# Kernel tuning notes

Measured on AMD Instinct MI355X. Metric: run time of the kernel, lower is better.

Reference implementation:

```python
import jax, jax.numpy as jnp
import numpy as np
from jax import lax

B, N, D, L, EDGE_H, NGNN = 8, 128, 256, 64, 64, 3


def setup_inputs() -> dict:
    key = jax.random.key(0)
    ks = iter(jax.random.split(key, 64))
    def nrm(shape, s=0.02):
        return jax.random.normal(next(ks), shape, jnp.float32) * s
    inp = {}
    inp["node_feats"] = jax.random.uniform(next(ks), (B, N, 11), jnp.float32)
    inp["edge_feats"] = jax.random.normal(next(ks), (B, N, N, 3), jnp.float32)
    inp["adj_mask"] = jax.random.randint(next(ks), (B, N, N), 0, 2).astype(bool)
    inp["layer_costs"] = jax.random.uniform(next(ks), (B, L), jnp.float32)
    inp["global_dynamic"] = jax.random.uniform(next(ks), (B, 2), jnp.float32)
    inp["p_node_w"] = nrm((11, D)); inp["p_node_b"] = jnp.zeros((D,), jnp.float32)
    inp["g_w1"] = nrm((NGNN, D + 3, EDGE_H)); inp["g_b1"] = jnp.zeros((NGNN, EDGE_H), jnp.float32)
    inp["g_w2"] = nrm((NGNN, EDGE_H, D)); inp["g_b2"] = jnp.zeros((NGNN, D), jnp.float32)
    inp["u_w1"] = nrm((NGNN, 3 * D, D)); inp["u_b1"] = jnp.zeros((NGNN, D), jnp.float32)
    inp["u_w2"] = nrm((NGNN, D, D)); inp["u_b2"] = jnp.zeros((NGNN, D), jnp.float32)
    inp["ln_g"] = jnp.ones((NGNN, D), jnp.float32); inp["ln_b"] = jnp.zeros((NGNN, D), jnp.float32)
    inp["conv_w"] = nrm((32, 1, 4)); inp["conv_b"] = jnp.zeros((32,), jnp.float32)
    inp["lp_w"] = nrm((32 * 31, D)); inp["lp_b"] = jnp.zeros((D,), jnp.float32)
    inp["q_w"] = nrm((2 * D + 2, D)); inp["q_b"] = jnp.zeros((D,), jnp.float32)
    inp["k_w"] = nrm((D, D)); inp["k_b"] = jnp.zeros((D,), jnp.float32)
    inp["s_w1"] = nrm((D + 2, D)); inp["s_b1"] = jnp.zeros((D,), jnp.float32)
    inp["s_w2"] = nrm((D, 1)); inp["s_b2"] = jnp.zeros((1,), jnp.float32)
    inp["v_w1"] = nrm((2 * D + 2, D)); inp["v_b1"] = jnp.zeros((D,), jnp.float32)
    inp["v_w2"] = nrm((D, 1)); inp["v_b2"] = jnp.zeros((1,), jnp.float32)
    return inp


def _ecgc(h, edge_feats, adj_bool, gw1, gb1, gw2, gb2, uw1, ub1, uw2, ub2, lng, lnb):
    Bh, Nn, Dd = h.shape
    # h_j: features of sender node j broadcast over receiver axis -> (B, N, N, D)
    h_j = jnp.broadcast_to(h[:, None, :, :], (Bh, Nn, Nn, Dd))
    gate_in = jnp.concatenate([h_j, edge_feats], axis=-1)            # (B,N,N,D+3)
    gates = jax.nn.sigmoid(jax.nn.relu(gate_in @ gw1 + gb1) @ gw2 + gb2)
    msg = gates * h_j                                                # (B,N,N,D)
    m = adj_bool.astype(h.dtype)[..., None]
    cnt = jnp.maximum(m.sum(axis=2), 1.0)                            # (B,N,1)
    agg_mean = (msg * m).sum(axis=2) / cnt                           # (B,N,D)
    agg_max = jnp.where(adj_bool[..., None], msg, -jnp.inf).max(axis=2)
    agg_max = jnp.where(jnp.isinf(agg_max), 0.0, agg_max)
    ui = jnp.concatenate([h, agg_mean, agg_max], axis=-1)            # (B,N,3D)
    x = h + (jax.nn.relu(ui @ uw1 + ub1) @ uw2 + ub2)
    mu = x.mean(-1, keepdims=True)
    var = ((x - mu) ** 2).mean(-1, keepdims=True)
    return (x - mu) * lax.rsqrt(var + 1e-5) * lng + lnb


def reference(node_feats, edge_feats, adj_mask, layer_costs, global_dynamic,
              p_node_w, p_node_b, g_w1, g_b1, g_w2, g_b2, u_w1, u_b1, u_w2, u_b2,
              ln_g, ln_b, conv_w, conv_b, lp_w, lp_b, q_w, q_b, k_w, k_b,
              s_w1, s_b1, s_w2, s_b2, v_w1, v_b1, v_w2, v_b2):
    # layer cost encoder: Conv1d(1,32,k=4,s=2) + ReLU, flatten, Linear
    le = lax.conv_general_dilated(layer_costs[:, None, :], conv_w, (2,), 'VALID',
                                  dimension_numbers=('NCH', 'OIH', 'NCH'))
    le = jax.nn.relu(le + conv_b[None, :, None])                     # (B,32,31)
    layer_embed = le.reshape(le.shape[0], -1) @ lp_w + lp_b          # (B,D)
    h = node_feats @ p_node_w + p_node_b                             # (B,N,D)
    for i in range(g_w1.shape[0]):
        h = _ecgc(h, edge_feats, adj_mask, g_w1[i], g_b1[i], g_w2[i], g_b2[i],
                  u_w1[i], u_b1[i], u_w2[i], u_b2[i], ln_g[i], ln_b[i])
    w = (node_feats[:, :, 0] * node_feats[:, :, 7])[..., None]       # (B,N,1)
    graph_embed = (w * h).sum(axis=1) / jnp.maximum(w.sum(axis=1), 1e-8)
    qi = jnp.concatenate([graph_embed, layer_embed, global_dynamic], axis=-1)
    query = qi @ q_w + q_b                                           # (B,D)
    keys = h @ k_w + k_b                                             # (B,N,D)
    device_scores = jnp.einsum('bnd,bd->bn', keys, query) / jnp.sqrt(jnp.float32(query.shape[-1]))
    si = jnp.concatenate([graph_embed, global_dynamic], axis=-1)
    stop_logit = jax.nn.relu(si @ s_w1 + s_b1) @ s_w2 + s_b2         # (B,1)
    all_logits = jnp.concatenate([device_scores, stop_logit], axis=1)
    value = jax.nn.relu(qi @ v_w1 + v_b1) @ v_w2 + v_b2              # (B,1)
    return all_logits, value, h
```

## Files before the change

kernel.cpp:

```cpp
#include <hip/hip_runtime.h>
#include <hip/hip_bf16.h>
#include <math.h>

#define BB 8
#define NN_ 128
#define DD 256
#define LL 64
#define EH 64
#define NG 3

typedef __attribute__((ext_vector_type(8))) short bs8;
typedef __attribute__((ext_vector_type(4))) float f4;

__device__ __forceinline__ short f2bf(float f) {
    __hip_bfloat16 h = __float2bfloat16(f);
    return *reinterpret_cast<short*>(&h);
}

__device__ __forceinline__ bs8 cvt8(const float* __restrict__ p) {
    bs8 r;
    #pragma unroll
    for (int i = 0; i < 8; ++i) r[i] = f2bf(p[i]);
    return r;
}

__device__ __forceinline__ float blockReduceSum(float v, float* sRed) {
    int tid = threadIdx.x;
    __syncthreads();
    sRed[tid] = v;
    __syncthreads();
    for (int s = 128; s > 0; s >>= 1) {
        if (tid < s) sRed[tid] += sRed[tid + s];
        __syncthreads();
    }
    return sRed[0];
}

__global__ __launch_bounds__(256) void k_prep(
    const float* __restrict__ uw1, const float* __restrict__ uw2,
    const float* __restrict__ gw2, const float* __restrict__ gw1,
    const float* __restrict__ kw, const unsigned char* __restrict__ adj,
    const float* __restrict__ lc, const float* __restrict__ cw,
    const float* __restrict__ cb, const float* __restrict__ lpw,
    unsigned short* __restrict__ w1t, unsigned short* __restrict__ w2t,
    unsigned short* __restrict__ g2t, unsigned short* __restrict__ g1t,
    unsigned short* __restrict__ kwt, int* __restrict__ mode,
    float* __restrict__ lpart)
{
    const int blk = blockIdx.x, tid = threadIdx.x;
    if (blk == 232) {
        __shared__ int sOff, sBig;
        if (tid == 0) { sOff = 0; sBig = 0; }
        __syncthreads();
        int off = 0, big = 0;
        #pragma unroll
        for (int k = 0; k < 4; ++k) {
            unsigned char v = adj[tid * 4 + k];
            if (v > 1) big = 1;
            if (k != 0 && v != 0) off = 1;
        }
        if (off) atomicOr(&sOff, 1);
        if (big) atomicOr(&sBig, 1);
        __syncthreads();
        if (tid == 0) mode[0] = sBig ? 2 : (sOff ? 0 : 1);
        return;
    }
    if (blk > 232) {
        const int lb = blk - 233;
        const int b = lb >> 5, kseg = (lb >> 2) & 7, c4 = lb & 3;
        const int d = tid & 63, ss = tid >> 6;
        __shared__ float sC[LL];
        __shared__ float sV[124];
        __shared__ float sP[4][64];
        if (tid < LL) sC[tid] = lc[b * LL + tid];
        __syncthreads();
        if (tid < 124) {
            int idx = kseg * 124 + tid;
            int c = idx / 31, t = idx - c * 31;
            float a = cb[c];
            #pragma unroll
            for (int k = 0; k < 4; ++k) a += sC[2 * t + k] * cw[c * 4 + k];
            sV[tid] = fmaxf(a, 0.f);
        }
        __syncthreads();
        float acc = 0.f;
        for (int k = ss; k < 124; k += 4)
            acc += sV[k] * lpw[(size_t)(kseg * 124 + k) * DD + c4 * 64 + d];
        sP[ss][d] = acc;
        __syncthreads();
        if (ss == 0)
            lpart[(b * 32 + kseg * 4 + c4) * 64 + d] = sP[0][d] + sP[1][d] + sP[2][d] + sP[3][d];
        return;
    }
    const float* src; unsigned short* dst; int K, kt, dt, srcw = 256;
    if (blk < 144)      { int l = blk / 48, t = blk % 48; kt = t >> 2; dt = t & 3;
                          src = uw1 + (size_t)l * 196608; dst = w1t + (size_t)l * 196608; K = 768; }
    else if (blk < 192) { int x = blk - 144, l = x / 16, t = x % 16; kt = t >> 2; dt = t & 3;
                          src = uw2 + (size_t)l * 65536; dst = w2t + (size_t)l * 65536; K = 256; }
    else if (blk < 204) { int x = blk - 192, l = x >> 2; kt = 0; dt = x & 3;
                          src = gw2 + (size_t)l * 16384; dst = g2t + (size_t)l * 16384; K = 64; }
    else if (blk < 216) { int x = blk - 204, l = x >> 2; kt = x & 3; dt = 0; srcw = 64;
                          src = gw1 + (size_t)l * 16576; dst = g1t + (size_t)l * 16384; K = 256; }
    else                { int x = blk - 216; kt = x >> 2; dt = x & 3;
                          src = kw; dst = kwt; K = 256; }
    __shared__ float sT[64][65];
    #pragma unroll
    for (int q = 0; q < 16; ++q) {
        int idx = q * 256 + tid, kk = idx >> 6, dd = idx & 63;
        sT[kk][dd] = src[(size_t)(kt * 64 + kk) * srcw + dt * 64 + dd];
    }
    __syncthreads();
    const int d = tid >> 2, kc = (tid & 3) * 16;
    unsigned short* drow = dst + (size_t)(dt * 64 + d) * K + kt * 64 + kc;
    #pragma unroll
    for (int i = 0; i < 16; ++i) drow[i] = (unsigned short)f2bf(sT[kc + i][d]);
}

__global__ __launch_bounds__(256) void k_npp(
    const float* __restrict__ nf, const float* __restrict__ pnw,
    const float* __restrict__ pnb,
    const unsigned short* __restrict__ g1t, const float* __restrict__ gb1,
    float* __restrict__ h, float* __restrict__ preg)
{
    const int tid = threadIdx.x, blk = blockIdx.x;
    const int row0 = blk * 16;
    const int lane = tid & 63, w = tid >> 6;
    const int lcol = lane & 15, lrow = lane >> 4;
    __shared__ float sF[16][12];
    __shared__ float sH[16][260];
    if (tid < 176) sF[tid / 11][tid % 11] = nf[(size_t)(row0 + tid / 11) * 11 + tid % 11];
    __syncthreads();
    float acc[16];
    {
        float bb = pnb[tid];
        #pragma unroll
        for (int rr = 0; rr < 16; ++rr) acc[rr] = bb;
    }
    #pragma unroll
    for (int f = 0; f < 11; ++f) {
        float wf = pnw[f * DD + tid];
        #pragma unroll
        for (int rr = 0; rr < 16; ++rr) acc[rr] += sF[rr][f] * wf;
    }
    #pragma unroll
    for (int rr = 0; rr < 16; ++rr) {
        sH[rr][tid] = acc[rr];
        h[(size_t)(row0 + rr) * DD + tid] = acc[rr];
    }
    __syncthreads();
    const unsigned short* bR = g1t + (size_t)(w * 16 + lcol) * 256;
    f4 a2 = {0.f, 0.f, 0.f, 0.f};
    #pragma unroll
    for (int ks = 0; ks < 8; ++ks) {
        int k0 = ks * 32 + lrow * 8;
        bs8 av = cvt8(&sH[lcol][k0]);
        bs8 bv = *(const bs8*)(bR + k0);
        a2 = __builtin_amdgcn_mfma_f32_16x16x32_bf16(av, bv, a2, 0, 0, 0);
    }
    const float gb = gb1[w * 16 + lcol];
    #pragma unroll
    for (int r = 0; r < 4; ++r)
        preg[(size_t)(row0 + lrow * 4 + r) * EH + w * 16 + lcol] = a2[r] + gb;
}

__global__ __launch_bounds__(256) void k_edge(
    const float* __restrict__ h, const float* __restrict__ preg,
    const float* __restrict__ edge, const void* __restrict__ adj,
    const int* __restrict__ mode,
    const float* __restrict__ gw1,
    const unsigned short* __restrict__ g2t,
    const float* __restrict__ gb2,
    float* __restrict__ agg_mean, float* __restrict__ agg_max)
{
    const int tid = threadIdx.x;
    const int bi = blockIdx.x;
    const int b = bi >> 7;
    const int lane = tid & 63, w = tid >> 6;
    const int lrow = lane >> 4, lcol = lane & 15;
    const int md = mode[0];

    __shared__ __align__(16) unsigned int sHid[4096];
    __shared__ float sWe[192];
    __shared__ float sE[384];
    __shared__ unsigned long long sMask[2];

    if (tid < 192) sWe[tid] = gw1[16384 + tid];
    const float* eB = edge + (size_t)bi * 384;
    for (int idx = tid; idx < 384; idx += 256) sE[idx] = eB[idx];
    if (tid < 128) {
        int mv;
        if (md == 1)      mv = ((const int*)adj)[(size_t)bi * NN_ + tid] != 0;
        else if (md == 2) mv = ((const float*)adj)[(size_t)bi * NN_ + tid] != 0.f;
        else              mv = ((const unsigned char*)adj)[(size_t)bi * NN_ + tid] != 0;
        unsigned long long bal = __ballot(mv);
        if ((tid & 63) == 0) sMask[tid >> 6] = bal;
    }
    __syncthreads();

    const float* pB = preg + (size_t)b * NN_ * EH;
    #pragma unroll
    for (int q = 0; q < 16; ++q) {
        int idx = q * 256 + tid;
        int j = idx >> 5, p = idx & 31;
        float2 pv = *(const float2*)(pB + j * EH + 2 * p);
        float e0 = sE[j * 3], e1 = sE[j * 3 + 1], e2 = sE[j * 3 + 2];
        int t0 = 2 * p, t1 = t0 + 1;
        float v0 = fmaxf(pv.x + e0 * sWe[t0] + e1 * sWe[64 + t0] + e2 * sWe[128 + t0], 0.f);
        float v1 = fmaxf(pv.y + e0 * sWe[t1] + e1 * sWe[64 + t1] + e2 * sWe[128 + t1], 0.f);
        unsigned int pk = (unsigned int)(unsigned short)f2bf(v0) |
                          ((unsigned int)(unsigned short)f2bf(v1) << 16);
        sHid[j * 32 + (p ^ ((j & 7) << 2))] = pk;
    }
    __syncthreads();

    const unsigned long long m0 = sMask[0], m1 = sMask[1];
    const float cntf = (float)(__popcll(m0) + __popcll(m1));

    bs8 bfr[4][2];
    float bg[4];
    #pragma unroll
    for (int nt = 0; nt < 4; ++nt) {
        int d = w * 64 + nt * 16 + lcol;
        bg[nt] = gb2[d];
        #pragma unroll
        for (int ks = 0; ks < 2; ++ks) {
            int k0 = ks * 32 + lrow * 8;
            bfr[nt][ks] = *(const bs8*)(g2t + (size_t)d * 64 + k0);
        }
    }

    const float* hB = h + (size_t)b * NN_ * DD;
    float vs[4] = {0.f, 0.f, 0.f, 0.f};
    float vm[4] = {-INFINITY, -INFINITY, -INFINITY, -INFINITY};

    #pragma unroll
    for (int pp = 0; pp < 2; ++pp) {
        f4 acc[4][4] = {};
        #pragma unroll
        for (int ks = 0; ks < 2; ++ks) {
            bs8 afr[4];
            #pragma unroll
            for (int m = 0; m < 4; ++m) {
                int j = pp * 64 + m * 16 + lcol;
                int k0 = ks * 32 + lrow * 8;
                afr[m] = *(const bs8*)(sHid + (j * 32 + ((k0 >> 1) ^ ((j & 7) << 2))));
            }
            #pragma unroll
            for (int m = 0; m < 4; ++m)
                #pragma unroll
                for (int nt = 0; nt < 4; ++nt)
                    acc[m][nt] = __builtin_amdgcn_mfma_f32_16x16x32_bf16(
                        afr[m], bfr[nt][ks], acc[m][nt], 0, 0, 0);
        }
        const unsigned long long mw = pp ? m1 : m0;
        #pragma unroll
        for (int m = 0; m < 4; ++m) {
            #pragma unroll
            for (int nt = 0; nt < 4; ++nt) {
                int dnt = w * 64 + nt * 16 + lcol;
                #pragma unroll
                for (int r = 0; r < 4; ++r) {
                    int bit = m * 16 + lrow * 4 + r;
                    float x = acc[m][nt][r] + bg[nt];
                    float g = __builtin_amdgcn_rcpf(1.0f + __expf(-x));
                    float msg = g * hB[(pp * 64 + bit) * DD + dnt];
                    int on = (int)((mw >> bit) & 1ULL);
                    vs[nt] += on ? msg : 0.f;
                    vm[nt] = fmaxf(vm[nt], on ? msg : -INFINITY);
                }
            }
        }
    }

    #pragma unroll
    for (int nt = 0; nt < 4; ++nt) {
        float s = vs[nt];
        s += __shfl_xor(s, 16); s += __shfl_xor(s, 32);
        vs[nt] = s;
        float m = vm[nt];
        m = fmaxf(m, __shfl_xor(m, 16)); m = fmaxf(m, __shfl_xor(m, 32));
        vm[nt] = m;
    }
    const int g = lrow;
    float ssel = (g == 0) ? vs[0] : (g == 1) ? vs[1] : (g == 2) ? vs[2] : vs[3];
    float msel = (g == 0) ? vm[0] : (g == 1) ? vm[1] : (g == 2) ? vm[2] : vm[3];
    const int d = w * 64 + lane;
    agg_mean[(size_t)bi * DD + d] = ssel / fmaxf(cntf, 1.f);
    agg_max[(size_t)bi * DD + d] = (cntf > 0.f) ? msel : 0.f;
}

__global__ __launch_bounds__(256) void k_updp(
    const float* __restrict__ h, const float* __restrict__ amean,
    const float* __restrict__ amax,
    const unsigned short* __restrict__ w1t,
    const float* __restrict__ ub1,
    const unsigned short* __restrict__ w2t,
    const float* __restrict__ ub2,
    const float* __restrict__ lng, const float* __restrict__ lnb,
    float* __restrict__ hout, float* __restrict__ out2,
    const unsigned short* __restrict__ g1tn, const float* __restrict__ gb1n,
    float* __restrict__ preg)
{
    const int tid = threadIdx.x;
    const int row0 = blockIdx.x * 4;
    const int lane = tid & 63, w = tid >> 6;
    const int lcol = lane & 15, lrow = lane >> 4;

    __shared__ __align__(16) unsigned int sX32[16 * 384];
    __shared__ __align__(16) unsigned short sH16[16 * 256];
    __shared__ float sRes[4][256];
    __shared__ float sOut[4][260];

    {
        const int j = w;
        const float* hR = h + (size_t)(row0 + j) * DD;
        const float* mR = amean + (size_t)(row0 + j) * DD;
        const float* xR = amax + (size_t)(row0 + j) * DD;
        #pragma unroll
        for (int q = 0; q < 6; ++q) {
            int p = lane + q * 64;
            int k = 2 * p;
            float2 v;
            if (k < 256)      { v = *(const float2*)(hR + k); sRes[j][k] = v.x; sRes[j][k + 1] = v.y; }
            else if (k < 512)   v = *(const float2*)(mR + (k - 256));
            else                v = *(const float2*)(xR + (k - 512));
            unsigned int pk = (unsigned int)(unsigned short)f2bf(v.x) |
                              ((unsigned int)(unsigned short)f2bf(v.y) << 16);
            sX32[j * 384 + (p ^ (j << 2))] = pk;
        }
    }
    __syncthreads();

    const char* sXb = (const char*)sX32;
    const unsigned short* w1r = w1t + (size_t)(w * 64 + lcol) * 768;
    f4 a0 = {0.f, 0.f, 0.f, 0.f}, a1 = a0, a2 = a0, a3 = a0;
    #pragma unroll 4
    for (int ks = 0; ks < 24; ++ks) {
        int k0 = ks * 32 + lrow * 8;
        bs8 av = *(const bs8*)(sXb + lcol * 1536 + ((((k0 >> 3) ^ (lcol & 7))) << 4));
        bs8 b0 = *(const bs8*)(w1r + k0);
        bs8 b1 = *(const bs8*)(w1r + 16 * 768 + k0);
        bs8 b2 = *(const bs8*)(w1r + 32 * 768 + k0);
        bs8 b3 = *(const bs8*)(w1r + 48 * 768 + k0);
        a0 = __builtin_amdgcn_mfma_f32_16x16x32_bf16(av, b0, a0, 0, 0, 0);
        a1 = __builtin_amdgcn_mfma_f32_16x16x32_bf16(av, b1, a1, 0, 0, 0);
        a2 = __builtin_amdgcn_mfma_f32_16x16x32_bf16(av, b2, a2, 0, 0, 0);
        a3 = __builtin_amdgcn_mfma_f32_16x16x32_bf16(av, b3, a3, 0, 0, 0);
    }
    if (lrow == 0) {
        #pragma unroll
        for (int nt = 0; nt < 4; ++nt) {
            int d = w * 64 + nt * 16 + lcol;
            float bb = ub1[d];
            f4 A = (nt == 0) ? a0 : (nt == 1) ? a1 : (nt == 2) ? a2 : a3;
            #pragma unroll
            for (int r = 0; r < 4; ++r) {
                float hv = fmaxf(A[r] + bb, 0.f);
                sH16[r * 256 + (d ^ (r << 3))] = (unsigned short)f2bf(hv);
            }
        }
    }
    __syncthreads();

    const unsigned short* w2r = w2t + (size_t)(w * 64 + lcol) * 256;
    f4 c0 = {0.f, 0.f, 0.f, 0.f}, c1 = c0, c2 = c0, c3 = c0;
    #pragma unroll
    for (int ks = 0; ks < 8; ++ks) {
        int k0 = ks * 32 + lrow * 8;
        bs8 av = *(const bs8*)((const char*)sH16 + lcol * 512 + ((((k0 >> 3) ^ (lcol & 7))) << 4));
        bs8 b0 = *(const bs8*)(w2r + k0);
        bs8 b1 = *(const bs8*)(w2r + 16 * 256 + k0);
        bs8 b2 = *(const bs8*)(w2r + 32 * 256 + k0);
        bs8 b3 = *(const bs8*)(w2r + 48 * 256 + k0);
        c0 = __builtin_amdgcn_mfma_f32_16x16x32_bf16(av, b0, c0, 0, 0, 0);
        c1 = __builtin_amdgcn_mfma_f32_16x16x32_bf16(av, b1, c1, 0, 0, 0);
        c2 = __builtin_amdgcn_mfma_f32_16x16x32_bf16(av, b2, c2, 0, 0, 0);
        c3 = __builtin_amdgcn_mfma_f32_16x16x32_bf16(av, b3, c3, 0, 0, 0);
    }
    if (lrow == 0) {
        #pragma unroll
        for (int nt = 0; nt < 4; ++nt) {
            int d = w * 64 + nt * 16 + lcol;
            float bb = ub2[d];
            f4 C = (nt == 0) ? c0 : (nt == 1) ? c1 : (nt == 2) ? c2 : c3;
            #pragma unroll
            for (int r = 0; r < 4; ++r)
                sOut[r][d] = C[r] + bb + sRes[r][d];
        }
    }
    __syncthreads();

    float xv[4], s = 0.f;
    #pragma unroll
    for (int q = 0; q < 4; ++q) { xv[q] = sOut[w][lane + 64 * q]; s += xv[q]; }
    #pragma unroll
    for (int off = 1; off < 64; off <<= 1) s += __shfl_xor(s, off);
    const float mu = s * (1.f / DD);
    float s2 = 0.f;
    #pragma unroll
    for (int q = 0; q < 4; ++q) { float d = xv[q] - mu; s2 += d * d; }
    #pragma unroll
    for (int off = 1; off < 64; off <<= 1) s2 += __shfl_xor(s2, off);
    const float inv = rsqrtf(s2 * (1.f / DD) + 1e-5f);
    #pragma unroll
    for (int q = 0; q < 4; ++q) {
        int c = lane + 64 * q;
        float res = (xv[q] - mu) * inv * lng[c] + lnb[c];
        hout[(size_t)(row0 + w) * DD + c] = res;
        if (out2) out2[(size_t)(row0 + w) * DD + c] = res;
        sOut[w][c] = res;
    }
    if (g1tn) {
        __syncthreads();
        const unsigned short* bR = g1tn + (size_t)(w * 16 + lcol) * 256;
        f4 p = {0.f, 0.f, 0.f, 0.f};
        #pragma unroll
        for (int ks = 0; ks < 8; ++ks) {
            int k0 = ks * 32 + lrow * 8;
            bs8 av = cvt8(&sOut[lcol & 3][k0]);
            bs8 bv = *(const bs8*)(bR + k0);
            p = __builtin_amdgcn_mfma_f32_16x16x32_bf16(av, bv, p, 0, 0, 0);
        }
        if (lrow == 0) {
            const float gb = gb1n[w * 16 + lcol];
            #pragma unroll
            for (int r = 0; r < 4; ++r)
                preg[(size_t)(row0 + r) * EH + w * 16 + lcol] = p[r] + gb;
        }
    }
}

__global__ __launch_bounds__(256) void k_gembed(
    const float* __restrict__ nf, const float* __restrict__ h, float* __restrict__ ge)
{
    const int b = blockIdx.x, tid = threadIdx.x;
    __shared__ float sW[NN_];
    __shared__ float sRed[256];
    if (tid < NN_) {
        const float* p = nf + ((size_t)b * NN_ + tid) * 11;
        sW[tid] = p[0] * p[7];
    }
    __syncthreads();
    float part = (tid < NN_) ? sW[tid] : 0.f;
    float wsum = blockReduceSum(part, sRed);
    const float* hb = h + (size_t)b * NN_ * DD + tid;
    float a0 = 0.f, a1 = 0.f, a2 = 0.f, a3 = 0.f;
    for (int n = 0; n < 32; ++n) {
        a0 += sW[n]      * hb[(size_t)n * DD];
        a1 += sW[n + 32] * hb[(size_t)(n + 32) * DD];
        a2 += sW[n + 64] * hb[(size_t)(n + 64) * DD];
        a3 += sW[n + 96] * hb[(size_t)(n + 96) * DD];
    }
    ge[b * DD + tid] = (a0 + a1 + a2 + a3) / fmaxf(wsum, 1e-8f);
}

__global__ __launch_bounds__(256) void k_hmm(
    const float* __restrict__ ge, const float* __restrict__ gd,
    const float* __restrict__ qw, const float* __restrict__ sw1,
    const float* __restrict__ vw1,
    const float* __restrict__ lpb, const float* __restrict__ lpart,
    float* __restrict__ part)
{
    const int blk = blockIdx.x;
    const int m = blk >> 5, kseg = (blk >> 2) & 7, c4 = blk & 3;
    const int tid = threadIdx.x;
    const int d = tid & 63, ks = tid >> 6;
    const int K = (m == 1) ? 258 : 514;
    const int kc = (m == 1) ? 33 : 65;
    const int k0 = kseg * kc;
    const int klen = min(k0 + kc, K) - k0;
    __shared__ float sX[8 * 66];
    __shared__ float sP[4][8][64];
    for (int idx = tid; idx < 8 * kc; idx += 256) {
        int bb = idx / kc, kk = idx % kc, k = k0 + kk;
        float v = 0.f;
        if (k < K) {
            if (m == 1) v = (k < 256) ? ge[bb * DD + k] : gd[bb * 2 + (k - 256)];
            else if (k < 256) v = ge[bb * DD + k];
            else if (k < 512) {
                int e = k - 256;
                v = lpb[e];
                #pragma unroll
                for (int s = 0; s < 8; ++s)
                    v += lpart[(bb * 32 + s * 4 + (e >> 6)) * 64 + (e & 63)];
            } else v = gd[bb * 2 + (k - 512)];
        }
        sX[bb * 66 + kk] = v;
    }
    __syncthreads();
    const float* W = (m == 0) ? qw : (m == 1) ? sw1 : vw1;
    const int dg = c4 * 64 + d;
    float acc[8] = {0.f, 0.f, 0.f, 0.f, 0.f, 0.f, 0.f, 0.f};
    for (int kk = ks; kk < klen; kk += 4) {
        float wv = W[(size_t)(k0 + kk) * DD + dg];
        #pragma unroll
        for (int bb = 0; bb < 8; ++bb) acc[bb] += sX[bb * 66 + kk] * wv;
    }
    #pragma unroll
    for (int bb = 0; bb < 8; ++bb) sP[ks][bb][d] = acc[bb];
    __syncthreads();
    for (int idx = tid; idx < 8 * 64; idx += 256) {
        int bb = idx >> 6, dd = idx & 63;
        float sum = sP[0][bb][dd] + sP[1][bb][dd] + sP[2][bb][dd] + sP[3][bb][dd];
        part[((m * 8 + kseg) * 8 + bb) * DD + c4 * 64 + dd] = sum;
    }
}

__global__ __launch_bounds__(256) void k_scr(
    const float* __restrict__ h, const unsigned short* __restrict__ kwt,
    const float* __restrict__ kb, const float* __restrict__ hpart,
    const float* __restrict__ qb,
    const float* __restrict__ sb1, const float* __restrict__ vb1,
    const float* __restrict__ sw2, const float* __restrict__ sb2,
    const float* __restrict__ vw2, const float* __restrict__ vb2,
    float* __restrict__ out)
{
    const int tid = threadIdx.x, blk = blockIdx.x;
    const int row0 = blk * 16, b = blk >> 3, chunk = blk & 7;
    const int lane = tid & 63, w = tid >> 6;
    const int lcol = lane & 15, lrow = lane >> 4;
    __shared__ float sQ[256];
    __shared__ float sPart[4][16];
    __shared__ float sRed[256];
    {
        float qv = qb[tid];
        #pragma unroll
        for (int kseg = 0; kseg < 8; ++kseg)
            qv += hpart[(size_t)(kseg * 8 + b) * DD + tid];
        sQ[tid] = qv;
    }
    __syncthreads();
    const float* aR = h + (size_t)(row0 + lcol) * DD;
    f4 acc[4] = {};
    #pragma unroll
    for (int ks = 0; ks < 8; ++ks) {
        int k0 = ks * 32 + lrow * 8;
        bs8 av = cvt8(aR + k0);
        #pragma unroll
        for (int nt = 0; nt < 4; ++nt) {
            bs8 bv = *(const bs8*)(kwt + (size_t)(w * 64 + nt * 16 + lcol) * 256 + k0);
            acc[nt] = __builtin_amdgcn_mfma_f32_16x16x32_bf16(av, bv, acc[nt], 0, 0, 0);
        }
    }
    float part[4] = {0.f, 0.f, 0.f, 0.f};
    #pragma unroll
    for (int nt = 0; nt < 4; ++nt) {
        int col = w * 64 + nt * 16 + lcol;
        float q = sQ[col], kv = kb[col];
        #pragma unroll
        for (int r = 0; r < 4; ++r) part[r] += (acc[nt][r] + kv) * q;
    }
    #pragma unroll
    for (int r = 0; r < 4; ++r) {
        float s = part[r];
        s += __shfl_xor(s, 1); s += __shfl_xor(s, 2);
        s += __shfl_xor(s, 4); s += __shfl_xor(s, 8);
        part[r] = s;
    }
    if (lcol == 0) {
        #pragma unroll
        for (int r = 0; r < 4; ++r) sPart[w][lrow * 4 + r] = part[r];
    }
    __syncthreads();
    if (tid < 16) {
        float s = sPart[0][tid] + sPart[1][tid] + sPart[2][tid] + sPart[3][tid];
        out[b * 129 + (row0 & (NN_ - 1)) + tid] = s * 0.0625f;
    }
    if (chunk == 0) {
        float s = sb1[tid], v = vb1[tid];
        #pragma unroll
        for (int kseg = 0; kseg < 8; ++kseg) {
            s += hpart[(size_t)((8 + kseg) * 8 + b) * DD + tid];
            v += hpart[(size_t)((16 + kseg) * 8 + b) * DD + tid];
        }
        s = fmaxf(s, 0.f); v = fmaxf(v, 0.f);
        float stop = blockReduceSum(s * sw2[tid], sRed);
        float val  = blockReduceSum(v * vw2[tid], sRed);
        if (tid == 0) {
            out[b * 129 + 128] = stop + sb2[0];
            out[1032 + b] = val + vb2[0];
        }
    }
}

extern "C" void kernel_launch(void* const* d_in, const int* in_sizes, int n_in,
                              void* d_out, int out_size, void* d_ws, size_t ws_size,
                              hipStream_t stream) {
    (void)in_sizes; (void)n_in; (void)out_size; (void)ws_size;
    const float* nf  = (const float*)d_in[0];
    const float* ef  = (const float*)d_in[1];
    const void*  adj = d_in[2];
    const float* lc  = (const float*)d_in[3];
    const float* gd  = (const float*)d_in[4];
    const float* pnw = (const float*)d_in[5];
    const float* pnb = (const float*)d_in[6];
    const float* gw1 = (const float*)d_in[7];
    const float* gb1 = (const float*)d_in[8];
    const float* gw2 = (const float*)d_in[9];
    const float* gb2 = (const float*)d_in[10];
    const float* uw1 = (const float*)d_in[11];
    const float* ub1 = (const float*)d_in[12];
    const float* uw2 = (const float*)d_in[13];
    const float* ub2 = (const float*)d_in[14];
    const float* lng = (const float*)d_in[15];
    const float* lnb = (const float*)d_in[16];
    const float* cw  = (const float*)d_in[17];
    const float* cb  = (const float*)d_in[18];
    const float* lpw = (const float*)d_in[19];
    const float* lpb = (const float*)d_in[20];
    const float* qw  = (const float*)d_in[21];
    const float* qb  = (const float*)d_in[22];
    const float* kw  = (const float*)d_in[23];
    const float* kb  = (const float*)d_in[24];
    const float* sw1 = (const float*)d_in[25];
    const float* sb1 = (const float*)d_in[26];
    const float* sw2 = (const float*)d_in[27];
    const float* sb2 = (const float*)d_in[28];
    const float* vw1 = (const float*)d_in[29];
    const float* vb1 = (const float*)d_in[30];
    const float* vw2 = (const float*)d_in[31];
    const float* vb2 = (const float*)d_in[32];

    float* ws = (float*)d_ws;
    float* h     = ws;
    float* preg  = ws + 262144;
    float* amean = ws + 327680;
    float* amax  = ws + 589824;
    float* ge    = ws + 851968;
    float* lpart = ws + 856064;
    float* hpart = ws + 872448;
    int*   mode  = (int*)(ws + 921600);
    unsigned short* uw1t = (unsigned short*)(ws + 921604);
    unsigned short* uw2t = (unsigned short*)(ws + 1216516);
    unsigned short* g2t  = (unsigned short*)(ws + 1314820);
    unsigned short* g1t  = (unsigned short*)(ws + 1339396);
    unsigned short* kwt  = (unsigned short*)(ws + 1363972);
    float* out   = (float*)d_out;

    k_prep<<<489, 256, 0, stream>>>(uw1, uw2, gw2, gw1, kw,
                                    (const unsigned char*)adj,
                                    lc, cw, cb, lpw,
                                    uw1t, uw2t, g2t, g1t, kwt, mode, lpart);
    k_npp<<<BB * NN_ / 16, 256, 0, stream>>>(nf, pnw, pnb, g1t, gb1, h, preg);
    for (int i = 0; i < NG; ++i) {
        const float* gw1i = gw1 + (size_t)i * 259 * EH;
        float* out2sel = (i == NG - 1) ? (out + 1040) : (float*)nullptr;
        const unsigned short* g1tn = (i < NG - 1) ? (g1t + (size_t)(i + 1) * 16384)
                                                  : (const unsigned short*)nullptr;
        const float* gb1n = (i < NG - 1) ? (gb1 + (i + 1) * EH) : (const float*)nullptr;
        k_edge<<<BB * NN_, 256, 0, stream>>>(h, preg, ef, adj, mode, gw1i,
                                             g2t + (size_t)i * 16384,
                                             gb2 + i * DD, amean, amax);
        k_updp<<<BB * NN_ / 4, 256, 0, stream>>>(h, amean, amax,
                                                 uw1t + (size_t)i * 196608, ub1 + i * DD,
                                                 uw2t + (size_t)i * 65536, ub2 + i * DD,
                                                 lng + i * DD, lnb + i * DD, h, out2sel,
                                                 g1tn, gb1n, preg);
    }
    k_gembed<<<BB, 256, 0, stream>>>(nf, h, ge);
    k_hmm<<<96, 256, 0, stream>>>(ge, gd, qw, sw1, vw1, lpb, lpart, hpart);
    k_scr<<<BB * NN_ / 16, 256, 0, stream>>>(h, kwt, kb, hpart, qb, sb1, vb1,
                                             sw2, sb2, vw2, vb2, out);
}
```

Before: 183.9 us.

## Fold node projection into prep kernel and graph-embed partials into update kernel

```diff
diff --git a/kernel.cpp b/kernel.cpp
--- a/kernel.cpp
+++ b/kernel.cpp
@@ -42,14 +42,18 @@
     const float* __restrict__ kw, const unsigned char* __restrict__ adj,
     const float* __restrict__ lc, const float* __restrict__ cw,
     const float* __restrict__ cb, const float* __restrict__ lpw,
+    const float* __restrict__ nf, const float* __restrict__ pnw,
+    const float* __restrict__ pnb, const float* __restrict__ gb1,
     unsigned short* __restrict__ w1t, unsigned short* __restrict__ w2t,
     unsigned short* __restrict__ g2t, unsigned short* __restrict__ g1t,
     unsigned short* __restrict__ kwt, int* __restrict__ mode,
-    float* __restrict__ lpart)
+    float* __restrict__ lpart, float* __restrict__ wsum,
+    float* __restrict__ h, float* __restrict__ preg)
 {
     const int blk = blockIdx.x, tid = threadIdx.x;
     if (blk == 232) {
         __shared__ int sOff, sBig;
+        __shared__ float sRedD[256];
         if (tid == 0) { sOff = 0; sBig = 0; }
         __syncthreads();
         int off = 0, big = 0;
@@ -63,6 +67,62 @@
         if (big) atomicOr(&sBig, 1);
         __syncthreads();
         if (tid == 0) mode[0] = sBig ? 2 : (sOff ? 0 : 1);
+        for (int bb = 0; bb < 8; ++bb) {
+            float v = 0.f;
+            if (tid < 128) {
+                const float* p = nf + (size_t)(bb * 128 + tid) * 11;
+                v = p[0] * p[7];
+            }
+            float s = blockReduceSum(v, sRedD);
+            if (tid == 0) wsum[bb] = s;
+        }
+        return;
+    }
+    if (blk >= 489) {
+        const int row0 = (blk - 489) * 16;
+        __shared__ float sF[16][12];
+        __shared__ float sCW[12][64];
+        if (tid < 176) sF[tid / 11][tid % 11] = nf[(size_t)(row0 + tid / 11) * 11 + tid % 11];
+        {
+            const int t = tid & 63, f0 = tid >> 6;
+            const float* r0p = pnw + (size_t)f0 * DD;
+            const float* r1p = pnw + (size_t)(f0 + 4) * DD;
+            const float* r2p = (f0 + 8 < 11) ? (pnw + (size_t)(f0 + 8) * DD) : pnb;
+            float a0 = 0.f, a1 = 0.f, a2 = 0.f;
+            for (int k = 0; k < 256; ++k) {
+                float g = gw1[k * EH + t];
+                a0 += r0p[k] * g; a1 += r1p[k] * g; a2 += r2p[k] * g;
+            }
+            if (f0 + 8 == 11) a2 += gb1[t];
+            sCW[f0][t] = a0; sCW[f0 + 4][t] = a1; sCW[f0 + 8][t] = a2;
+        }
+        __syncthreads();
+        float acc[16];
+        {
+            float bb = pnb[tid];
+            #pragma unroll
+            for (int rr = 0; rr < 16; ++rr) acc[rr] = bb;
+        }
+        #pragma unroll
+        for (int f = 0; f < 11; ++f) {
+            float wf = pnw[f * DD + tid];
+            #pragma unroll
+            for (int rr = 0; rr < 16; ++rr) acc[rr] += sF[rr][f] * wf;
+        }
+        #pragma unroll
+        for (int rr = 0; rr < 16; ++rr)
+            h[(size_t)(row0 + rr) * DD + tid] = acc[rr];
+        {
+            const int t = tid & 63, r0 = tid >> 6;
+            #pragma unroll
+            for (int q = 0; q < 4; ++q) {
+                int rr = r0 * 4 + q;
+                float a = sCW[11][t];
+                #pragma unroll
+                for (int f = 0; f < 11; ++f) a += sF[rr][f] * sCW[f][t];
+                preg[(size_t)(row0 + rr) * EH + t] = a;
+            }
+        }
         return;
     }
     if (blk > 232) {
@@ -114,53 +174,6 @@
     unsigned short* drow = dst + (size_t)(dt * 64 + d) * K + kt * 64 + kc;
     #pragma unroll
     for (int i = 0; i < 16; ++i) drow[i] = (unsigned short)f2bf(sT[kc + i][d]);
-}
-
-__global__ __launch_bounds__(256) void k_npp(
-    const float* __restrict__ nf, const float* __restrict__ pnw,
-    const float* __restrict__ pnb,
-    const unsigned short* __restrict__ g1t, const float* __restrict__ gb1,
-    float* __restrict__ h, float* __restrict__ preg)
-{
-    const int tid = threadIdx.x, blk = blockIdx.x;
-    const int row0 = blk * 16;
-    const int lane = tid & 63, w = tid >> 6;
-    const int lcol = lane & 15, lrow = lane >> 4;
-    __shared__ float sF[16][12];
-    __shared__ float sH[16][260];
-    if (tid < 176) sF[tid / 11][tid % 11] = nf[(size_t)(row0 + tid / 11) * 11 + tid % 11];
-    __syncthreads();
-    float acc[16];
-    {
-        float bb = pnb[tid];
-        #pragma unroll
-        for (int rr = 0; rr < 16; ++rr) acc[rr] = bb;
-    }
-    #pragma unroll
-    for (int f = 0; f < 11; ++f) {
-        float wf = pnw[f * DD + tid];
-        #pragma unroll
-        for (int rr = 0; rr < 16; ++rr) acc[rr] += sF[rr][f] * wf;
-    }
-    #pragma unroll
-    for (int rr = 0; rr < 16; ++rr) {
-        sH[rr][tid] = acc[rr];
-        h[(size_t)(row0 + rr) * DD + tid] = acc[rr];
-    }
-    __syncthreads();
-    const unsigned short* bR = g1t + (size_t)(w * 16 + lcol) * 256;
-    f4 a2 = {0.f, 0.f, 0.f, 0.f};
-    #pragma unroll
-    for (int ks = 0; ks < 8; ++ks) {
-        int k0 = ks * 32 + lrow * 8;
-        bs8 av = cvt8(&sH[lcol][k0]);
-        bs8 bv = *(const bs8*)(bR + k0);
-        a2 = __builtin_amdgcn_mfma_f32_16x16x32_bf16(av, bv, a2, 0, 0, 0);
-    }
-    const float gb = gb1[w * 16 + lcol];
-    #pragma unroll
-    for (int r = 0; r < 4; ++r)
-        preg[(size_t)(row0 + lrow * 4 + r) * EH + w * 16 + lcol] = a2[r] + gb;
 }
 
 __global__ __launch_bounds__(256) void k_edge(
@@ -291,7 +304,7 @@
 
 __global__ __launch_bounds__(256) void k_updp(
     const float* __restrict__ h, const float* __restrict__ amean,
-    const float* __restrict__ amax,
+    const float* __restrict__ amax, const float* __restrict__ nf,
     const unsigned short* __restrict__ w1t,
     const float* __restrict__ ub1,
     const unsigned short* __restrict__ w2t,
@@ -299,7 +312,7 @@
     const float* __restrict__ lng, const float* __restrict__ lnb,
     float* __restrict__ hout, float* __restrict__ out2,
     const unsigned short* __restrict__ g1tn, const float* __restrict__ gb1n,
-    float* __restrict__ preg)
+    float* __restrict__ preg, float* __restrict__ gpart)
 {
     const int tid = threadIdx.x;
     const int row0 = blockIdx.x * 4;
@@ -310,7 +323,12 @@
     __shared__ __align__(16) unsigned short sH16[16 * 256];
     __shared__ float sRes[4][256];
     __shared__ float sOut[4][260];
-
+    __shared__ float sWr[4];
+
+    if (tid < 4) {
+        const float* p = nf + (size_t)(row0 + tid) * 11;
+        sWr[tid] = p[0] * p[7];
+    }
     {
         const int j = w;
         const float* hR = h + (size_t)(row0 + j) * DD;
@@ -410,8 +428,8 @@
         if (out2) out2[(size_t)(row0 + w) * DD + c] = res;
         sOut[w][c] = res;
     }
+    __syncthreads();
     if (g1tn) {
-        __syncthreads();
         const unsigned short* bR = g1tn + (size_t)(w * 16 + lcol) * 256;
         f4 p = {0.f, 0.f, 0.f, 0.f};
         #pragma unroll
@@ -422,40 +440,21 @@
             p = __builtin_amdgcn_mfma_f32_16x16x32_bf16(av, bv, p, 0, 0, 0);
         }
         if (lrow == 0) {
-            const float gb = gb1n[w * 16 + lcol];
+            const float gb_ = gb1n[w * 16 + lcol];
             #pragma unroll
             for (int r = 0; r < 4; ++r)
-                preg[(size_t)(row0 + r) * EH + w * 16 + lcol] = p[r] + gb;
-        }
-    }
-}
-
-__global__ __launch_bounds__(256) void k_gembed(
-    const float* __restrict__ nf, const float* __restrict__ h, float* __restrict__ ge)
-{
-    const int b = blockIdx.x, tid = threadIdx.x;
-    __shared__ float sW[NN_];
-    __shared__ float sRed[256];
-    if (tid < NN_) {
-        const float* p = nf + ((size_t)b * NN_ + tid) * 11;
-        sW[tid] = p[0] * p[7];
-    }
-    __syncthreads();
-    float part = (tid < NN_) ? sW[tid] : 0.f;
-    float wsum = blockReduceSum(part, sRed);
-    const float* hb = h + (size_t)b * NN_ * DD + tid;
-    float a0 = 0.f, a1 = 0.f, a2 = 0.f, a3 = 0.f;
-    for (int n = 0; n < 32; ++n) {
-        a0 += sW[n]      * hb[(size_t)n * DD];
-        a1 += sW[n + 32] * hb[(size_t)(n + 32) * DD];
-        a2 += sW[n + 64] * hb[(size_t)(n + 64) * DD];
-        a3 += sW[n + 96] * hb[(size_t)(n + 96) * DD];
-    }
-    ge[b * DD + tid] = (a0 + a1 + a2 + a3) / fmaxf(wsum, 1e-8f);
+                preg[(size_t)(row0 + r) * EH + w * 16 + lcol] = p[r] + gb_;
+        }
+    } else {
+        float g = sWr[0] * sOut[0][tid] + sWr[1] * sOut[1][tid] +
+                  sWr[2] * sOut[2][tid] + sWr[3] * sOut[3][tid];
+        gpart[(size_t)blockIdx.x * DD + tid] = g;
+    }
 }
 
 __global__ __launch_bounds__(256) void k_hmm(
-    const float* __restrict__ ge, const float* __restrict__ gd,
+    const float* __restrict__ gpart, const float* __restrict__ wsum,
+    const float* __restrict__ gd,
     const float* __restrict__ qw, const float* __restrict__ sw1,
     const float* __restrict__ vw1,
     const float* __restrict__ lpb, const float* __restrict__ lpart,
@@ -475,15 +474,23 @@
         int bb = idx / kc, kk = idx % kc, k = k0 + kk;
         float v = 0.f;
         if (k < K) {
-            if (m == 1) v = (k < 256) ? ge[bb * DD + k] : gd[bb * 2 + (k - 256)];
-            else if (k < 256) v = ge[bb * DD + k];
-            else if (k < 512) {
+            if (k < 256) {
+                float s = 0.f;
+                #pragma unroll 8
+                for (int t = 0; t < 32; ++t)
+                    s += gpart[(size_t)(bb * 32 + t) * DD + k];
+                v = s / fmaxf(wsum[bb], 1e-8f);
+            } else if (m == 1) {
+                v = gd[bb * 2 + (k - 256)];
+            } else if (k < 512) {
                 int e = k - 256;
                 v = lpb[e];
                 #pragma unroll
                 for (int s = 0; s < 8; ++s)
                     v += lpart[(bb * 32 + s * 4 + (e >> 6)) * 64 + (e & 63)];
-            } else v = gd[bb * 2 + (k - 512)];
+            } else {
+                v = gd[bb * 2 + (k - 512)];
+            }
         }
         sX[bb * 66 + kk] = v;
     }
@@ -626,22 +633,23 @@
     float* preg  = ws + 262144;
     float* amean = ws + 327680;
     float* amax  = ws + 589824;
-    float* ge    = ws + 851968;
-    float* lpart = ws + 856064;
-    float* hpart = ws + 872448;
-    int*   mode  = (int*)(ws + 921600);
-    unsigned short* uw1t = (unsigned short*)(ws + 921604);
-    unsigned short* uw2t = (unsigned short*)(ws + 1216516);
-    unsigned short* g2t  = (unsigned short*)(ws + 1314820);
-    unsigned short* g1t  = (unsigned short*)(ws + 1339396);
-    unsigned short* kwt  = (unsigned short*)(ws + 1363972);
+    float* lpart = ws + 851968;
+    float* hpart = ws + 868352;
+    float* gpart = ws + 917504;
+    float* wsum  = ws + 983040;
+    int*   mode  = (int*)(ws + 983048);
+    unsigned short* uw1t = (unsigned short*)(ws + 983052);
+    unsigned short* uw2t = (unsigned short*)(ws + 1277964);
+    unsigned short* g2t  = (unsigned short*)(ws + 1376268);
+    unsigned short* g1t  = (unsigned short*)(ws + 1400844);
+    unsigned short* kwt  = (unsigned short*)(ws + 1425420);
     float* out   = (float*)d_out;
 
-    k_prep<<<489, 256, 0, stream>>>(uw1, uw2, gw2, gw1, kw,
+    k_prep<<<553, 256, 0, stream>>>(uw1, uw2, gw2, gw1, kw,
                                     (const unsigned char*)adj,
-                                    lc, cw, cb, lpw,
-                                    uw1t, uw2t, g2t, g1t, kwt, mode, lpart);
-    k_npp<<<BB * NN_ / 16, 256, 0, stream>>>(nf, pnw, pnb, g1t, gb1, h, preg);
+                                    lc, cw, cb, lpw, nf, pnw, pnb, gb1,
+                                    uw1t, uw2t, g2t, g1t, kwt, mode, lpart, wsum,
+                                    h, preg);
     for (int i = 0; i < NG; ++i) {
         const float* gw1i = gw1 + (size_t)i * 259 * EH;
         float* out2sel = (i == NG - 1) ? (out + 1040) : (float*)nullptr;
@@ -651,14 +659,13 @@
         k_edge<<<BB * NN_, 256, 0, stream>>>(h, preg, ef, adj, mode, gw1i,
                                              g2t + (size_t)i * 16384,
                                              gb2 + i * DD, amean, amax);
-        k_updp<<<BB * NN_ / 4, 256, 0, stream>>>(h, amean, amax,
+        k_updp<<<BB * NN_ / 4, 256, 0, stream>>>(h, amean, amax, nf,
                                                  uw1t + (size_t)i * 196608, ub1 + i * DD,
                                                  uw2t + (size_t)i * 65536, ub2 + i * DD,
                                                  lng + i * DD, lnb + i * DD, h, out2sel,
-                                                 g1tn, gb1n, preg);
-    }
-    k_gembed<<<BB, 256, 0, stream>>>(nf, h, ge);
-    k_hmm<<<96, 256, 0, stream>>>(ge, gd, qw, sw1, vw1, lpb, lpart, hpart);
+                                                 g1tn, gb1n, preg, gpart);
+    }
+    k_hmm<<<96, 256, 0, stream>>>(gpart, wsum, gd, qw, sw1, vw1, lpb, lpart, hpart);
     k_scr<<<BB * NN_ / 16, 256, 0, stream>>>(h, kwt, kb, hpart, qb, sb1, vb1,
                                              sw2, sb2, vw2, vb2, out);
 }
```

Result: no change. 186.0 us (+1.2%).
